# Kernel optimization log

Measured on AMD Instinct MI355X. Metric: run time of the kernel, lower is better.

The kernel has to match this reference:

```python
import jax, jax.numpy as jnp
import numpy as np

NUM_HEADS = 16
D_K = 64
BATCH_SIZE = 64
NUM_EDGES = 32768


def setup_inputs() -> dict:
    key = jax.random.key(0)
    k1, k2, k3, k4 = jax.random.split(key, 4)
    global_query = jax.random.normal(k1, (NUM_HEADS, BATCH_SIZE, D_K), dtype=jnp.float32)
    local_key = jax.random.normal(k2, (NUM_HEADS, NUM_EDGES, D_K), dtype=jnp.float32)
    local_value = jax.random.normal(k3, (NUM_HEADS, NUM_EDGES, D_K), dtype=jnp.float32)
    batch = jnp.sort(jax.random.randint(k4, (NUM_EDGES,), 0, BATCH_SIZE, dtype=jnp.int64))
    return {"global_query": global_query, "local_key": local_key,
            "local_value": local_value, "batch": batch}


def reference(global_query, local_key, local_value, batch):
    # global_query: [h, b, d]; local_key/value: [h, e, d]; batch: [e] segment ids
    num_heads, batch_size, d_k = global_query.shape
    # seg[b, e] = True iff edge e belongs to graph b
    seg = batch[None, :] == jnp.arange(batch_size, dtype=batch.dtype)[:, None]  # [b, e]
    # NOTE: original module does NOT scale by sqrt(d_k) despite its name
    scores = jnp.einsum('hbd,hed->hbe', global_query, local_key)  # [h, b, e]
    # per-segment softmax: out-of-segment entries get -inf -> exactly 0 weight,
    # matching the original which only softmaxes over edges with batch == i
    masked = jnp.where(seg[None, :, :], scores, -jnp.inf)
    attn = jax.nn.softmax(masked, axis=-1)  # [h, b, e]; zeros outside segment
    output = jnp.einsum('hbe,hed->hbd', attn, local_value)  # [h, b, d]
    return output, attn
```

## Files before the change

kernel.cpp:

```cpp
#include <hip/hip_runtime.h>
#include <math.h>

#define NH 16
#define NB 64
#define DK 64
#define NE 32768
#define LDS_CAP 2048

typedef float vf4 __attribute__((ext_vector_type(4)));


__global__ void seg_bounds_kernel(const int* __restrict__ batch, int* __restrict__ bounds) {
    int e = blockIdx.x * 256 + threadIdx.x;
    if (e >= NE) return;
    int be = batch[e];
    if (e == 0) {
        for (int b = 0; b <= be; ++b) bounds[b] = 0;
    } else {
        int bp = batch[e - 1];
        for (int b = bp + 1; b <= be; ++b) bounds[b] = e;
    }
    if (e == NE - 1) {
        for (int b = be + 1; b <= NB; ++b) bounds[b] = NE;
    }
}

__global__ __launch_bounds__(256) void fused_kernel(
    const float* __restrict__ Q,
    const float* __restrict__ K,
    const float* __restrict__ V,
    const int*   __restrict__ bounds,
    float* __restrict__ out,
    float* __restrict__ attn)
{
    const int task = blockIdx.x;
    const int h    = task >> 6;
    const int b    = task & (NB - 1);
    const int tid  = threadIdx.x;
    const int wave = tid >> 6;
    const int lane = tid & 63;
    const int j    = lane >> 4;
    const int c    = lane & 15;

    const int start = bounds[b];
    const int end   = bounds[b + 1];
    const int S     = end - start;
    const bool single = (S <= LDS_CAP);

    __shared__ float qs[DK];
    __shared__ float ssc[LDS_CAP];
    __shared__ float sm[4], sl[4];
    __shared__ float bM, bInv;
    __shared__ float red[4][16][4];

    if (tid < DK) qs[tid] = Q[((size_t)h * NB + b) * DK + tid];
    __syncthreads();

    const float4  qc  = ((const float4*)qs)[c];
    const float4* K4  = (const float4*)(K + (size_t)h * NE * DK);
    const float4* V4  = (const float4*)(V + (size_t)h * NE * DK);
    float* arow = attn + ((size_t)h * NB + b) * NE;

    float m = -INFINITY, l = 0.f;
    int e = start + wave * 4;
    for (; e + 115 < end; e += 128) {
        float4 kv[8];
        #pragma unroll
        for (int u = 0; u < 8; ++u)
            kv[u] = K4[(size_t)(e + 16 * u + j) * (DK / 4) + c];
        float s[8];
        #pragma unroll
        for (int u = 0; u < 8; ++u) {
            float t = fmaf(kv[u].x, qc.x, fmaf(kv[u].y, qc.y,
                      fmaf(kv[u].z, qc.z, kv[u].w * qc.w)));
            #pragma unroll
            for (int off = 1; off < 16; off <<= 1)
                t += __shfl_xor(t, off);
            s[u] = t;
            if (single && c == 0) ssc[e + 16 * u + j - start] = t;
        }
        float mx = fmaxf(fmaxf(fmaxf(s[0], s[1]), fmaxf(s[2], s[3])),
                         fmaxf(fmaxf(s[4], s[5]), fmaxf(s[6], s[7])));
        const float nm = fmaxf(m, mx);
        float sum = 0.f;
        #pragma unroll
        for (int u = 0; u < 8; ++u) sum += __expf(s[u] - nm);
        l = l * __expf(m - nm) + sum;
        m = nm;
    }
    for (; e < end; e += 16) {
        const int  ej    = e + j;
        const bool valid = ej < end;
        const int  el    = valid ? ej : end - 1;
        const float4 kv = K4[(size_t)el * (DK / 4) + c];
        float t = fmaf(kv.x, qc.x, fmaf(kv.y, qc.y, fmaf(kv.z, qc.z, kv.w * qc.w)));
        #pragma unroll
        for (int off = 1; off < 16; off <<= 1)
            t += __shfl_xor(t, off);
        if (valid) {
            if (single && c == 0) ssc[ej - start] = t;
            float nm = fmaxf(m, t);
            l = l * __expf(m - nm) + __expf(t - nm);
            m = nm;
        }
    }

    #pragma unroll
    for (int off = 16; off < 64; off <<= 1) {
        float om = __shfl_xor(m, off);
        float ol = __shfl_xor(l, off);
        float nm = fmaxf(m, om);
        float t1 = (l  > 0.f) ? l  * __expf(m  - nm) : 0.f;
        float t2 = (ol > 0.f) ? ol * __expf(om - nm) : 0.f;
        m = nm; l = t1 + t2;
    }
    if (lane == 0) { sm[wave] = m; sl[wave] = l; }
    __syncthreads();
    if (tid == 0) {
        float M = -INFINITY;
        #pragma unroll
        for (int w = 0; w < 4; ++w) M = fmaxf(M, sm[w]);
        float L = 0.f;
        #pragma unroll
        for (int w = 0; w < 4; ++w) L += (sl[w] > 0.f) ? sl[w] * __expf(sm[w] - M) : 0.f;
        bM = M; bInv = (L > 0.f) ? 1.f / L : 0.f;
    }
    __syncthreads();
    const float M   = bM;
    const float inv = bInv;

    {
        vf4 z4 = (vf4)(0.f);
        vf4* arow4 = (vf4*)arow;
        const int zs = start >> 2;
        const int ze = (end + 3) >> 2;
        for (int i = tid; i < zs; i += 256) arow4[i] = z4;
        for (int i = ze + tid; i < NE / 4; i += 256) arow4[i] = z4;
        if (tid == 0) {
            for (int p = (zs << 2); p < start; ++p) arow[p] = 0.f;
        } else if (tid == 1) {
            for (int p = end; p < (ze << 2); ++p) arow[p] = 0.f;
        }
    }

    float4 acc = make_float4(0.f, 0.f, 0.f, 0.f);

    if (single) {
        for (int ep = start + tid; ep < end; ep += 256)
            arow[ep] = __expf(ssc[ep - start] - M) * inv;

        int ev = start + wave * 4;
        for (; ev + 115 < end; ev += 128) {
            float4 v[8]; float p[8];
            #pragma unroll
            for (int u = 0; u < 8; ++u) {
                const int ej = ev + 16 * u + j;
                p[u] = ssc[ej - start];
                v[u] = V4[(size_t)ej * (DK / 4) + c];
            }
            #pragma unroll
            for (int u = 0; u < 8; ++u) {
                const float pe = __expf(p[u] - M) * inv;
                acc.x = fmaf(pe, v[u].x, acc.x);
                acc.y = fmaf(pe, v[u].y, acc.y);
                acc.z = fmaf(pe, v[u].z, acc.z);
                acc.w = fmaf(pe, v[u].w, acc.w);
            }
        }
        for (; ev < end; ev += 16) {
            const int  ej    = ev + j;
            const bool valid = ej < end;
            const int  el    = valid ? ej : end - 1;
            const float pe = valid ? __expf(ssc[el - start] - M) * inv : 0.f;
            const float4 v = V4[(size_t)el * (DK / 4) + c];
            acc.x = fmaf(pe, v.x, acc.x);
            acc.y = fmaf(pe, v.y, acc.y);
            acc.z = fmaf(pe, v.z, acc.z);
            acc.w = fmaf(pe, v.w, acc.w);
        }
    } else {
        for (int cs = start; cs < end; cs += LDS_CAP) {
            const int ce = (cs + LDS_CAP < end) ? cs + LDS_CAP : end;
            __syncthreads();
            for (int ek = cs + wave * 4; ek < ce; ek += 16) {
                const int  ej    = ek + j;
                const bool valid = ej < ce;
                const int  el    = valid ? ej : ce - 1;
                const float4 kv = K4[(size_t)el * (DK / 4) + c];
                float t = fmaf(kv.x, qc.x, fmaf(kv.y, qc.y, fmaf(kv.z, qc.z, kv.w * qc.w)));
                #pragma unroll
                for (int off = 1; off < 16; off <<= 1)
                    t += __shfl_xor(t, off);
                if (valid && c == 0) ssc[el - cs] = t;
            }
            __syncthreads();
            for (int ep = cs + tid; ep < ce; ep += 256)
                arow[ep] = __expf(ssc[ep - cs] - M) * inv;
            for (int ev = cs + wave * 4; ev < ce; ev += 16) {
                const int  ej    = ev + j;
                const bool valid = ej < ce;
                const int  el    = valid ? ej : ce - 1;
                const float pe = valid ? __expf(ssc[el - cs] - M) * inv : 0.f;
                const float4 v = V4[(size_t)el * (DK / 4) + c];
                acc.x = fmaf(pe, v.x, acc.x);
                acc.y = fmaf(pe, v.y, acc.y);
                acc.z = fmaf(pe, v.z, acc.z);
                acc.w = fmaf(pe, v.w, acc.w);
            }
        }
    }

    #pragma unroll
    for (int off = 16; off < 64; off <<= 1) {
        acc.x += __shfl_xor(acc.x, off);
        acc.y += __shfl_xor(acc.y, off);
        acc.z += __shfl_xor(acc.z, off);
        acc.w += __shfl_xor(acc.w, off);
    }
    if (lane < 16) {
        red[wave][c][0] = acc.x;
        red[wave][c][1] = acc.y;
        red[wave][c][2] = acc.z;
        red[wave][c][3] = acc.w;
    }
    __syncthreads();
    if (tid < DK) {
        const int cc = tid >> 2, comp = tid & 3;
        float r = red[0][cc][comp] + red[1][cc][comp]
                + red[2][cc][comp] + red[3][cc][comp];
        out[((size_t)h * NB + b) * DK + tid] = r;
    }
}

extern "C" void kernel_launch(void* const* d_in, const int* in_sizes, int n_in,
                              void* d_out, int out_size, void* d_ws, size_t ws_size,
                              hipStream_t stream) {
    const float* Q     = (const float*)d_in[0];
    const float* K     = (const float*)d_in[1];
    const float* V     = (const float*)d_in[2];
    const int*   batch = (const int*)d_in[3];

    float* out  = (float*)d_out;
    float* attn = out + (size_t)NH * NB * DK;

    int*   bounds = (int*)d_ws;

    seg_bounds_kernel<<<NE / 256, 256, 0, stream>>>(batch, bounds);

    fused_kernel<<<NH * NB, 256, 0, stream>>>(Q, K, V, bounds, out, attn);
}
```

Before: 324.2 us.

## Double-buffer K and V tiles into LDS via global_load_lds and defer attn writes

Replaces the direct per-thread global loads of K and V in the single-chunk path with a double-buffered pipeline. Each step copies a 48-row tile straight into LDS using global_load_lds while the previous tile is consumed, and the V prefetch begins before the softmax statistics are combined. The zero-fill and attn-row writes move to the end of the kernel so they no longer sit between the two streaming passes. In exchange the kernel uses more LDS, adds a block barrier per chunk, and the inner loop now processes one row per step instead of eight unrolled rows, which may reduce memory-level parallelism.

```diff
diff --git a/kernel.cpp b/kernel.cpp
--- a/kernel.cpp
+++ b/kernel.cpp
@@ -6,8 +6,14 @@
 #define DK 64
 #define NE 32768
 #define LDS_CAP 2048
+#define CHUNK 48
+#define ROWB 256
 
 typedef float vf4 __attribute__((ext_vector_type(4)));
+
+#define GLDS(g, l) \
+  __builtin_amdgcn_global_load_lds((__attribute__((address_space(1))) const void*)(g), \
+                                   (__attribute__((address_space(3))) void*)(l), 16, 0, 0)
 
 
 __global__ void seg_bounds_kernel(const int* __restrict__ batch, int* __restrict__ bounds) {
@@ -22,6 +28,17 @@
     }
     if (e == NE - 1) {
         for (int b = be + 1; b <= NB; ++b) bounds[b] = NE;
+    }
+}
+
+__device__ __forceinline__ void stage_rows(const char* __restrict__ gbase, float* lb,
+                                           int e0, int wave, int lane) {
+    const size_t head_max = (size_t)NE * ROWB - 16;
+    #pragma unroll
+    for (int i = 0; i < 3; ++i) {
+        size_t off = (size_t)e0 * ROWB + (size_t)(wave * 3 + i) * 1024 + (size_t)lane * 16;
+        if (off > head_max) off = head_max;
+        GLDS(gbase + off, (char*)lb + (wave * 3 + i) * 1024);
     }
 }
 
@@ -46,63 +63,53 @@
     const int end   = bounds[b + 1];
     const int S     = end - start;
     const bool single = (S <= LDS_CAP);
-
-    __shared__ float qs[DK];
-    __shared__ float ssc[LDS_CAP];
+    const int nc    = (S + CHUNK - 1) / CHUNK;
+
+    __shared__ __align__(16) float kbuf[2][CHUNK * DK];
+    __shared__ __align__(16) float ssc[LDS_CAP];
+    __shared__ __align__(16) float qs[DK];
     __shared__ float sm[4], sl[4];
     __shared__ float bM, bInv;
     __shared__ float red[4][16][4];
 
     if (tid < DK) qs[tid] = Q[((size_t)h * NB + b) * DK + tid];
-    __syncthreads();
-
-    const float4  qc  = ((const float4*)qs)[c];
-    const float4* K4  = (const float4*)(K + (size_t)h * NE * DK);
-    const float4* V4  = (const float4*)(V + (size_t)h * NE * DK);
+
+    const char* gK = (const char*)K + (size_t)h * NE * ROWB;
+    const char* gV = (const char*)V + (size_t)h * NE * ROWB;
+    const float4* K4 = (const float4*)(K + (size_t)h * NE * DK);
+    const float4* V4 = (const float4*)(V + (size_t)h * NE * DK);
     float* arow = attn + ((size_t)h * NB + b) * NE;
 
+    if (nc > 0) stage_rows(gK, kbuf[0], start, wave, lane);
+    __syncthreads();
+
+    const float4 qc = ((const float4*)qs)[c];
+
     float m = -INFINITY, l = 0.f;
-    int e = start + wave * 4;
-    for (; e + 115 < end; e += 128) {
-        float4 kv[8];
+    int cur = 0;
+    for (int t = 0; t < nc; ++t) {
+        const int e0 = start + t * CHUNK;
+        if (t + 1 < nc) stage_rows(gK, kbuf[cur ^ 1], e0 + CHUNK, wave, lane);
+        const float4* kb4 = (const float4*)kbuf[cur];
         #pragma unroll
-        for (int u = 0; u < 8; ++u)
-            kv[u] = K4[(size_t)(e + 16 * u + j) * (DK / 4) + c];
-        float s[8];
-        #pragma unroll
-        for (int u = 0; u < 8; ++u) {
-            float t = fmaf(kv[u].x, qc.x, fmaf(kv[u].y, qc.y,
-                      fmaf(kv[u].z, qc.z, kv[u].w * qc.w)));
+        for (int s = 0; s < 3; ++s) {
+            const int r = s * 16 + wave * 4 + j;
+            const int e = e0 + r;
+            const bool valid = e < end;
+            const float4 kv = kb4[r * 16 + c];
+            float t2 = fmaf(kv.x, qc.x, fmaf(kv.y, qc.y, fmaf(kv.z, qc.z, kv.w * qc.w)));
             #pragma unroll
             for (int off = 1; off < 16; off <<= 1)
-                t += __shfl_xor(t, off);
-            s[u] = t;
-            if (single && c == 0) ssc[e + 16 * u + j - start] = t;
-        }
-        float mx = fmaxf(fmaxf(fmaxf(s[0], s[1]), fmaxf(s[2], s[3])),
-                         fmaxf(fmaxf(s[4], s[5]), fmaxf(s[6], s[7])));
-        const float nm = fmaxf(m, mx);
-        float sum = 0.f;
-        #pragma unroll
-        for (int u = 0; u < 8; ++u) sum += __expf(s[u] - nm);
-        l = l * __expf(m - nm) + sum;
-        m = nm;
-    }
-    for (; e < end; e += 16) {
-        const int  ej    = e + j;
-        const bool valid = ej < end;
-        const int  el    = valid ? ej : end - 1;
-        const float4 kv = K4[(size_t)el * (DK / 4) + c];
-        float t = fmaf(kv.x, qc.x, fmaf(kv.y, qc.y, fmaf(kv.z, qc.z, kv.w * qc.w)));
-        #pragma unroll
-        for (int off = 1; off < 16; off <<= 1)
-            t += __shfl_xor(t, off);
-        if (valid) {
-            if (single && c == 0) ssc[ej - start] = t;
-            float nm = fmaxf(m, t);
-            l = l * __expf(m - nm) + __expf(t - nm);
-            m = nm;
-        }
+                t2 += __shfl_xor(t2, off);
+            if (valid) {
+                if (single && c == 0) ssc[e - start] = t2;
+                float nm = fmaxf(m, t2);
+                l = l * __expf(m - nm) + __expf(t2 - nm);
+                m = nm;
+            }
+        }
+        __syncthreads();
+        cur ^= 1;
     }
 
     #pragma unroll
@@ -116,6 +123,9 @@
     }
     if (lane == 0) { sm[wave] = m; sl[wave] = l; }
     __syncthreads();
+
+    if (single && nc > 0) stage_rows(gV, kbuf[0], start, wave, lane);
+
     if (tid == 0) {
         float M = -INFINITY;
         #pragma unroll
@@ -129,54 +139,29 @@
     const float M   = bM;
     const float inv = bInv;
 
-    {
-        vf4 z4 = (vf4)(0.f);
-        vf4* arow4 = (vf4*)arow;
-        const int zs = start >> 2;
-        const int ze = (end + 3) >> 2;
-        for (int i = tid; i < zs; i += 256) arow4[i] = z4;
-        for (int i = ze + tid; i < NE / 4; i += 256) arow4[i] = z4;
-        if (tid == 0) {
-            for (int p = (zs << 2); p < start; ++p) arow[p] = 0.f;
-        } else if (tid == 1) {
-            for (int p = end; p < (ze << 2); ++p) arow[p] = 0.f;
-        }
-    }
-
     float4 acc = make_float4(0.f, 0.f, 0.f, 0.f);
 
     if (single) {
-        for (int ep = start + tid; ep < end; ep += 256)
-            arow[ep] = __expf(ssc[ep - start] - M) * inv;
-
-        int ev = start + wave * 4;
-        for (; ev + 115 < end; ev += 128) {
-            float4 v[8]; float p[8];
+        cur = 0;
+        for (int t = 0; t < nc; ++t) {
+            const int e0 = start + t * CHUNK;
+            if (t + 1 < nc) stage_rows(gV, kbuf[cur ^ 1], e0 + CHUNK, wave, lane);
+            const float4* vb4 = (const float4*)kbuf[cur];
             #pragma unroll
-            for (int u = 0; u < 8; ++u) {
-                const int ej = ev + 16 * u + j;
-                p[u] = ssc[ej - start];
-                v[u] = V4[(size_t)ej * (DK / 4) + c];
-            }
-            #pragma unroll
-            for (int u = 0; u < 8; ++u) {
-                const float pe = __expf(p[u] - M) * inv;
-                acc.x = fmaf(pe, v[u].x, acc.x);
-                acc.y = fmaf(pe, v[u].y, acc.y);
-                acc.z = fmaf(pe, v[u].z, acc.z);
-                acc.w = fmaf(pe, v[u].w, acc.w);
-            }
-        }
-        for (; ev < end; ev += 16) {
-            const int  ej    = ev + j;
-            const bool valid = ej < end;
-            const int  el    = valid ? ej : end - 1;
-            const float pe = valid ? __expf(ssc[el - start] - M) * inv : 0.f;
-            const float4 v = V4[(size_t)el * (DK / 4) + c];
-            acc.x = fmaf(pe, v.x, acc.x);
-            acc.y = fmaf(pe, v.y, acc.y);
-            acc.z = fmaf(pe, v.z, acc.z);
-            acc.w = fmaf(pe, v.w, acc.w);
+            for (int s = 0; s < 3; ++s) {
+                const int r = s * 16 + wave * 4 + j;
+                const int e = e0 + r;
+                const bool valid = e < end;
+                const int  si = valid ? (e - start) : 0;
+                const float pe = valid ? __expf(ssc[si] - M) * inv : 0.f;
+                const float4 v = vb4[r * 16 + c];
+                acc.x = fmaf(pe, v.x, acc.x);
+                acc.y = fmaf(pe, v.y, acc.y);
+                acc.z = fmaf(pe, v.z, acc.z);
+                acc.w = fmaf(pe, v.w, acc.w);
+            }
+            __syncthreads();
+            cur ^= 1;
         }
     } else {
         for (int cs = start; cs < end; cs += LDS_CAP) {
@@ -187,11 +172,11 @@
                 const bool valid = ej < ce;
                 const int  el    = valid ? ej : ce - 1;
                 const float4 kv = K4[(size_t)el * (DK / 4) + c];
-                float t = fmaf(kv.x, qc.x, fmaf(kv.y, qc.y, fmaf(kv.z, qc.z, kv.w * qc.w)));
+                float t2 = fmaf(kv.x, qc.x, fmaf(kv.y, qc.y, fmaf(kv.z, qc.z, kv.w * qc.w)));
                 #pragma unroll
                 for (int off = 1; off < 16; off <<= 1)
-                    t += __shfl_xor(t, off);
-                if (valid && c == 0) ssc[el - cs] = t;
+                    t2 += __shfl_xor(t2, off);
+                if (valid && c == 0) ssc[el - cs] = t2;
             }
             __syncthreads();
             for (int ep = cs + tid; ep < ce; ep += 256)
@@ -230,6 +215,24 @@
                 + red[2][cc][comp] + red[3][cc][comp];
         out[((size_t)h * NB + b) * DK + tid] = r;
     }
+
+    if (single) {
+        for (int ep = start + tid; ep < end; ep += 256)
+            arow[ep] = __expf(ssc[ep - start] - M) * inv;
+    }
+    {
+        vf4 z4 = (vf4)(0.f);
+        vf4* arow4 = (vf4*)arow;
+        const int zs = start >> 2;
+        const int ze = (end + 3) >> 2;
+        for (int i = tid; i < zs; i += 256) arow4[i] = z4;
+        for (int i = ze + tid; i < NE / 4; i += 256) arow4[i] = z4;
+        if (tid == 0) {
+            for (int p = (zs << 2); p < start; ++p) arow[p] = 0.f;
+        } else if (tid == 1) {
+            for (int p = end; p < (ze << 2); ++p) arow[p] = 0.f;
+        }
+    }
 }
 
 extern "C" void kernel_launch(void* const* d_in, const int* in_sizes, int n_in,
```

After: 332.4 us. +2.5%, slower.
